# Performance work log

Measured on AMD Instinct MI355X. Metric: run time of the kernel, lower is better.

Reference implementation:

```python
import jax, jax.numpy as jnp
import numpy as np

B, S, D = 2, 512, 2048          # batch, seq, hidden
H, Dh = 16, 128                 # heads, head_dim
E, K, G, TG = 8, 2, 2, 1        # experts, top_k, n_group, topk_group
I, IS = 1024, 1024              # routed / shared expert intermediate
ROUTED_SCALE = 2.5
EPS = 1e-6
ROPE_THETA = 10000.0


def setup_inputs() -> dict:
    key = jax.random.key(0)
    ks = jax.random.split(key, 13)
    p = lambda k, shape, s=0.02: jax.random.normal(k, shape, jnp.float32) * s
    return {
        "hidden_states": jax.random.normal(ks[0], (B, S, D), jnp.float32),
        "ln1_w": jnp.ones((D,), jnp.float32),
        "ln2_w": jnp.ones((D,), jnp.float32),
        "wq": p(ks[1], (D, H * Dh)),
        "wk": p(ks[2], (D, H * Dh)),
        "wv": p(ks[3], (D, H * Dh)),
        "wo": p(ks[4], (H * Dh, D)),
        "gate_w": p(ks[5], (E, D)),
        "gate_bias": p(ks[6], (E,), 0.1),
        "w_gate": p(ks[7], (E, D, I)),
        "w_up": p(ks[8], (E, D, I)),
        "w_down": p(ks[9], (E, I, D)),
        "sw_gate": p(ks[10], (D, IS)),
        "sw_up": p(ks[11], (D, IS)),
        "sw_down": p(ks[12], (IS, D)),
    }


def _rmsnorm(x, w):
    var = jnp.mean(x * x, axis=-1, keepdims=True)
    return x * jax.lax.rsqrt(var + EPS) * w


def _rope_cos_sin(seq_len):
    inv_freq = 1.0 / (ROPE_THETA ** (jnp.arange(0, Dh, 2, dtype=jnp.float32) / Dh))
    ang = jnp.arange(seq_len, dtype=jnp.float32)[:, None] * inv_freq  # [S, Dh/2]
    return jnp.cos(ang)[None, :, None, :], jnp.sin(ang)[None, :, None, :]


def _apply_rope(x, cos, sin):
    x1, x2 = jnp.split(x, 2, axis=-1)
    return jnp.concatenate([x1 * cos - x2 * sin, x2 * cos + x1 * sin], axis=-1)


def _attention(x, wq, wk, wv, wo):
    q = (x @ wq).reshape(B, S, H, Dh)
    k = (x @ wk).reshape(B, S, H, Dh)
    v = (x @ wv).reshape(B, S, H, Dh)
    cos, sin = _rope_cos_sin(S)
    q = _apply_rope(q, cos, sin)
    k = _apply_rope(k, cos, sin)
    scores = jnp.einsum('bqhd,bkhd->bhqk', q, k) * (1.0 / np.sqrt(Dh).astype(np.float32))
    causal = jnp.tril(jnp.ones((S, S), bool))
    scores = jnp.where(causal, scores, jnp.finfo(scores.dtype).min)
    attn = jax.nn.softmax(scores, axis=-1)
    out = jnp.einsum('bhqk,bkhd->bqhd', attn, v).reshape(B, S, H * Dh)
    return out @ wo


def _moe(x, gate_w, gate_bias, w_gate, w_up, w_down, sw_gate, sw_up, sw_down):
    # x: [T, D]. noaux_tc grouped top-k routing (DeepSeek-V3 style).
    T = x.shape[0]
    logits = x @ gate_w.T                      # [T, E]
    scores = jax.nn.sigmoid(logits)
    sc = scores + gate_bias                    # selection scores with correction bias
    grp = sc.reshape(T, G, E // G)
    group_scores = jnp.sum(jax.lax.top_k(grp, 2)[0], axis=-1)  # top-2 sum per group [T,G]
    _, gidx = jax.lax.top_k(group_scores, TG)
    gmask = jnp.zeros((T, G), bool).at[jnp.arange(T)[:, None], gidx].set(True)
    emask = jnp.broadcast_to(gmask[:, :, None], (T, G, E // G)).reshape(T, E)
    masked = jnp.where(emask, sc, -jnp.inf)
    _, idx = jax.lax.top_k(masked, K)          # [T, K] expert ids
    w = jnp.take_along_axis(scores, idx, axis=-1)
    w = w / jnp.sum(w, axis=-1, keepdims=True)  # norm_topk_prob=True
    # dense combine weights [T, E] (zero except K entries per token)
    cw = jnp.zeros((T, E), x.dtype).at[jnp.arange(T)[:, None], idx].add(w)

    def body(acc, xs):
        wg, wu, wd, cwe = xs
        y = (jax.nn.silu(x @ wg) * (x @ wu)) @ wd  # SiluAndMul gated MLP
        return acc + cwe[:, None] * y, None

    routed, _ = jax.lax.scan(body, jnp.zeros_like(x), (w_gate, w_up, w_down, cw.T))
    shared = (jax.nn.silu(x @ sw_gate) * (x @ sw_up)) @ sw_down
    return routed * ROUTED_SCALE + shared


def reference(hidden_states, ln1_w, ln2_w, wq, wk, wv, wo, gate_w, gate_bias,
              w_gate, w_up, w_down, sw_gate, sw_up, sw_down):
    h = hidden_states
    h = h + _attention(_rmsnorm(h, ln1_w), wq, wk, wv, wo)
    x = _rmsnorm(h, ln2_w).reshape(B * S, D)
    moe_out = _moe(x, gate_w, gate_bias, w_gate, w_up, w_down,
                   sw_gate, sw_up, sw_down).reshape(B, S, D)
    return h + moe_out
```

## Files before the change

kernel.cpp:

```cpp
#include <hip/hip_runtime.h>

typedef __bf16 bf16x4 __attribute__((ext_vector_type(4)));
typedef __bf16 bf16x8 __attribute__((ext_vector_type(8)));
typedef float  f32x4  __attribute__((ext_vector_type(4)));

#define THREADS 256
constexpr int BK = 32, BKP = 40;

constexpr size_t MB = 1024*1024;
constexpr size_t oH2    = 0;
constexpr size_t oXB2   = 8*MB;
constexpr size_t oRT    = 12*MB;
constexpr size_t oWQKVT = 16*MB;
constexpr size_t oWQKVL = 40*MB;
constexpr size_t oWOT   = 64*MB;
constexpr size_t oWOL   = 72*MB;
constexpr size_t oXN1   = 80*MB;
constexpr size_t oXN1L  = 84*MB;
constexpr size_t oQKV   = 88*MB;
constexpr size_t oSCF   = 112*MB;
constexpr size_t oQKS   = 144*MB;
constexpr size_t oQKSL  = 152*MB;
constexpr size_t oVT    = 16*MB;
constexpr size_t oVTL   = 20*MB;
constexpr size_t oATT   = 24*MB;
constexpr size_t oPB    = 40*MB;
constexpr size_t oPBL2  = 88*MB;
constexpr size_t oWGUT  = 16*MB;
constexpr size_t oWDT   = 80*MB;
constexpr size_t oSGUT  = 112*MB;
constexpr size_t oSDT   = 120*MB;
constexpr size_t oGU    = 124*MB;
constexpr size_t oHB    = 140*MB;
constexpr size_t oY     = 144*MB;
constexpr size_t oSGU   = 16*MB;
constexpr size_t oSHB   = 24*MB;
constexpr size_t oSDB   = 26*MB;
constexpr size_t oEIDX = oRT;
constexpr size_t oEW   = oRT + 8192;
constexpr size_t oSLOT = oRT + 16384;
constexpr size_t oLIST = oRT + 24576;
constexpr size_t oCNT  = oRT + 32768;
constexpr size_t oOFF  = oRT + 33024;
constexpr size_t oCUR  = oRT + 33280;

__device__ __forceinline__ bf16x8 bzero8() {
  bf16x8 z;
#pragma unroll
  for (int j = 0; j < 8; ++j) z[j] = (__bf16)0.f;
  return z;
}

template<int OM>
__global__ void transpose_kernel(const float* __restrict__ in, __bf16* __restrict__ out,
                                 int ldin, int ldout, int zlo,
                                 long inBH, long inBL, long outB, long plane) {
  __shared__ float tile[64][65];
  int z = blockIdx.z;
  const float* inp = in + (long)(z / zlo) * inBH + (long)(z % zlo) * inBL;
  __bf16* outp = out + (long)z * outB;
  int r0 = blockIdx.y * 64, c0 = blockIdx.x * 64;
  int tid = threadIdx.x;
#pragma unroll
  for (int i = 0; i < 4; ++i) {
    int lin = tid + i * 256;
    int r = lin >> 4, c4 = (lin & 15) << 2;
    f32x4 v = *(const f32x4*)(inp + (long)(r0 + r) * ldin + c0 + c4);
    tile[r][c4] = v[0]; tile[r][c4+1] = v[1]; tile[r][c4+2] = v[2]; tile[r][c4+3] = v[3];
  }
  __syncthreads();
#pragma unroll
  for (int i = 0; i < 4; ++i) {
    int lin = tid + i * 256;
    int oR = lin >> 4, oC4 = (lin & 15) << 2;
    bf16x4 hi, lo;
#pragma unroll
    for (int j = 0; j < 4; ++j) {
      float v = tile[oC4 + j][oR];
      hi[j] = (__bf16)v;
      if constexpr (OM == 2) lo[j] = (__bf16)(v - (float)hi[j]);
    }
    __bf16* dst = outp + (long)(c0 + oR) * ldout + r0 + oC4;
    *(bf16x4*)dst = hi;
    if constexpr (OM == 2) *(bf16x4*)(dst + plane) = lo;
  }
}

template<int MODE, int SP, bool RESID, bool CAUSAL, bool KTRI, int TBM = 128, int TBN = 128>
__global__ __launch_bounds__(256, 2)
void gemm_kernel(const void* __restrict__ Av, const void* __restrict__ Bv, float* __restrict__ C,
                 const float* __restrict__ Rres,
                 int M, int N, int K, int lda, int ldb, int ldc,
                 int zlo, long aHi, long aLo, long bHi, long bLo, long cHi, long cLo,
                 long aPlane, long bPlane,
                 const int* __restrict__ counts, const int* __restrict__ offsets,
                 const int* __restrict__ gather) {
  const int n0 = blockIdx.x * TBN;
  const int m0 = blockIdx.y * TBM;
  const int z  = blockIdx.z;
  if (CAUSAL && n0 > m0) return;

  const float*  Af = (const float*)Av;
  const __bf16* Ah = (const __bf16*)Av;
  const __bf16* Bh = (const __bf16*)Bv;

  int mcount; int rowbase = 0;
  long aoff = 0, boff = 0, coff = 0;
  if constexpr (MODE == 0) {
    mcount = M;
    int zh = z / zlo, zl = z % zlo;
    aoff = (long)zh*aHi + (long)zl*aLo;
    boff = (long)zh*bHi + (long)zl*bLo;
    coff = (long)zh*cHi + (long)zl*cLo;
  } else {
    mcount = counts[z];
    rowbase = offsets[z];
    if (m0 >= mcount) return;
    boff = (long)z*bHi;
  }

  constexpr bool TRI = (SP != 0);
  constexpr int ABUF = TBM*BKP;
  constexpr int BBUF = TBN*BKP;
  constexpr int WTM = TBM/2, WTN = TBN/2;
  constexpr int MI = WTM/16, MJ = WTN/16;
  __shared__ __align__(16) __bf16 As[(TRI?2:1)*ABUF];
  __shared__ __align__(16) __bf16 Bs[(TRI?2:1)*BBUF];

  const int tid = threadIdx.x;
  const int lane = tid & 63, wave = tid >> 6;
  const int wm = wave >> 1, wn = wave & 1;
  const int lq = lane >> 4, lr = lane & 15;

  int kend = K;
  if (KTRI) { int ke = m0 + TBM; kend = ke < K ? ke : K; }

  f32x4 acc[MI][MJ] = {};

  constexpr int NAF = (SP==1) ? TBM/32 : 1;
  constexpr int NAH = (SP!=1) ? TBM/64 : 1;
  constexpr int NB  = TBN/64;
  f32x4  arf[NAF];
  bf16x8 arh[NAH], arl[NAH];
  bf16x8 brh[NB],  brl[NB];

  auto loadAB = [&](int kk) {
    if constexpr (SP == 1) {
#pragma unroll
      for (int it = 0; it < NAF; ++it) {
        int lin = tid + it*THREADS;
        int row = lin >> 3, c4 = (lin & 7) << 2;
        int gr = m0 + row;
        f32x4 zv; zv[0]=0.f; zv[1]=0.f; zv[2]=0.f; zv[3]=0.f;
        arf[it] = (gr < mcount) ? *(const f32x4*)(Af + aoff + (long)gr*lda + kk + c4) : zv;
      }
    } else {
#pragma unroll
      for (int it = 0; it < NAH; ++it) {
        int lin = tid + it*THREADS;
        int row = lin >> 2, c8 = (lin & 3) << 3;
        int gr = m0 + row;
        arh[it] = bzero8();
        if constexpr (SP == 2) arl[it] = bzero8();
        if (gr < mcount) {
          long arow;
          if constexpr (MODE == 1) arow = gather[rowbase + gr];
          else if constexpr (MODE == 2) arow = rowbase + gr;
          else arow = gr;
          const __bf16* p = Ah + aoff + arow*(long)lda + kk + c8;
          arh[it] = *(const bf16x8*)p;
          if constexpr (SP == 2) arl[it] = *(const bf16x8*)(p + aPlane);
        }
      }
    }
#pragma unroll
    for (int it = 0; it < NB; ++it) {
      int lin = tid + it*THREADS;
      int row = lin >> 2, c8 = (lin & 3) << 3;
      const __bf16* p = Bh + boff + (long)(n0+row)*ldb + kk + c8;
      brh[it] = *(const bf16x8*)p;
      if constexpr (TRI) brl[it] = *(const bf16x8*)(p + bPlane);
    }
  };

  auto writeAB = [&]() {
    if constexpr (SP == 1) {
#pragma unroll
      for (int it = 0; it < NAF; ++it) {
        int lin = tid + it*THREADS;
        int row = lin >> 3, c4 = (lin & 7) << 2;
        bf16x4 hi, lo;
#pragma unroll
        for (int j = 0; j < 4; ++j) {
          hi[j] = (__bf16)arf[it][j];
          lo[j] = (__bf16)(arf[it][j] - (float)hi[j]);
        }
        *(bf16x4*)(As + row*BKP + c4) = hi;
        *(bf16x4*)(As + ABUF + row*BKP + c4) = lo;
      }
    } else {
#pragma unroll
      for (int it = 0; it < NAH; ++it) {
        int lin = tid + it*THREADS;
        int row = lin >> 2, c8 = (lin & 3) << 3;
        *(bf16x8*)(As + row*BKP + c8) = arh[it];
        if constexpr (SP == 2) *(bf16x8*)(As + ABUF + row*BKP + c8) = arl[it];
      }
    }
#pragma unroll
    for (int it = 0; it < NB; ++it) {
      int lin = tid + it*THREADS;
      int row = lin >> 2, c8 = (lin & 3) << 3;
      *(bf16x8*)(Bs + row*BKP + c8) = brh[it];
      if constexpr (TRI) *(bf16x8*)(Bs + BBUF + row*BKP + c8) = brl[it];
    }
  };

  loadAB(0);
  writeAB();
  __syncthreads();

  for (int k0 = 0; k0 < kend; k0 += BK) {
    const bool hn = (k0 + BK < kend);
    if (hn) loadAB(k0 + BK);

    bf16x8 fa[MI], fal[MI];
    const __bf16* ap = As + (wm*WTM + lr)*BKP + lq*8;
    const __bf16* bp = Bs + (wn*WTN + lr)*BKP + lq*8;
#pragma unroll
    for (int i = 0; i < MI; ++i) {
      fa[i] = *(const bf16x8*)(ap + i*16*BKP);
      if constexpr (TRI) fal[i] = *(const bf16x8*)(ap + ABUF + i*16*BKP);
    }
#pragma unroll
    for (int j = 0; j < MJ; ++j) {
      bf16x8 fb = *(const bf16x8*)(bp + j*16*BKP);
      if constexpr (TRI) {
        bf16x8 fbl = *(const bf16x8*)(bp + BBUF + j*16*BKP);
#pragma unroll
        for (int i = 0; i < MI; ++i) {
          acc[i][j] = __builtin_amdgcn_mfma_f32_16x16x32_bf16(fa[i],  fbl, acc[i][j], 0, 0, 0);
          acc[i][j] = __builtin_amdgcn_mfma_f32_16x16x32_bf16(fal[i], fb,  acc[i][j], 0, 0, 0);
          acc[i][j] = __builtin_amdgcn_mfma_f32_16x16x32_bf16(fa[i],  fb,  acc[i][j], 0, 0, 0);
        }
      } else {
#pragma unroll
        for (int i = 0; i < MI; ++i)
          acc[i][j] = __builtin_amdgcn_mfma_f32_16x16x32_bf16(fa[i], fb, acc[i][j], 0, 0, 0);
      }
    }

    if (hn) {
      __syncthreads();
      writeAB();
      __syncthreads();
    }
  }

#pragma unroll
  for (int i = 0; i < MI; ++i) {
#pragma unroll
    for (int rg = 0; rg < 4; ++rg) {
      int lrow = wm*WTM + i*16 + lq*4 + rg;
      int gr = m0 + lrow;
      if (gr < mcount) {
        long crow = coff + (long)(rowbase + gr)*ldc;
#pragma unroll
        for (int j = 0; j < MJ; ++j) {
          int col = n0 + wn*WTN + j*16 + lr;
          float val = acc[i][j][rg];
          if constexpr (RESID) val += Rres[(long)gr*ldc + col];
          C[crow + col] = val;
        }
      }
    }
  }
}

template<int OM>
__global__ void rmsnorm_kernel(const float* __restrict__ x, const float* __restrict__ w,
                               __bf16* __restrict__ out, long plane) {
  const int row = blockIdx.x;
  const float* xr = x + (long)row * 2048;
  float ss = 0.f;
  for (int d = threadIdx.x; d < 2048; d += 256) { float v = xr[d]; ss += v*v; }
  __shared__ float red[4];
  int lane = threadIdx.x & 63, wave = threadIdx.x >> 6;
#pragma unroll
  for (int off = 32; off; off >>= 1) ss += __shfl_down(ss, off, 64);
  if (lane == 0) red[wave] = ss;
  __syncthreads();
  float tot = red[0] + red[1] + red[2] + red[3];
  float rs = rsqrtf(tot * (1.f/2048.f) + 1e-6f);
  __bf16* orow = out + (long)row * 2048;
  for (int d = threadIdx.x; d < 2048; d += 256) {
    float v = xr[d]*rs*w[d];
    __bf16 h = (__bf16)v;
    orow[d] = h;
    if constexpr (OM == 2) orow[d + plane] = (__bf16)(v - (float)h);
  }
}

__global__ void rope_split_kernel(const float* __restrict__ qkv, __bf16* __restrict__ o, long plane) {
  int tid = blockIdx.x*256 + threadIdx.x;
  int i = tid & 63;
  int th = tid >> 6;
  int h = th & 15;
  int t = th >> 4;
  int s = t & 511;
  long ib = (long)t*6144 + h*128;
  long ob = (long)t*4096 + h*128;
  float inv = 1.f / powf(10000.f, (float)i * (1.f/64.f));
  float ang = (float)s * inv;
  float c = cosf(ang), sn = sinf(ang);
  float q1 = qkv[ib+i], q2 = qkv[ib+64+i];
  float r1 = q1*c - q2*sn, r2 = q2*c + q1*sn;
  __bf16 h1 = (__bf16)r1, h2v = (__bf16)r2;
  o[ob+i] = h1;            o[ob+i+plane] = (__bf16)(r1 - (float)h1);
  o[ob+64+i] = h2v;        o[ob+64+i+plane] = (__bf16)(r2 - (float)h2v);
  float k1 = qkv[ib+2048+i], k2 = qkv[ib+2048+64+i];
  float s1 = k1*c - k2*sn, s2 = k2*c + k1*sn;
  __bf16 g1 = (__bf16)s1, g2 = (__bf16)s2;
  o[ob+2048+i] = g1;       o[ob+2048+i+plane] = (__bf16)(s1 - (float)g1);
  o[ob+2048+64+i] = g2;    o[ob+2048+64+i+plane] = (__bf16)(s2 - (float)g2);
}

__global__ void softmax_kernel(const float* __restrict__ sc, __bf16* __restrict__ p, long plane) {
  int r = blockIdx.x & 511;
  long bh = blockIdx.x >> 9;
  const float scale = 0.08838834764831845f;
  long base = (bh*512 + r)*512;
  int c0 = threadIdx.x, c1 = threadIdx.x + 256;
  float v0 = (c0 <= r) ? sc[base+c0]*scale : -3.0e38f;
  float v1 = (c1 <= r) ? sc[base+c1]*scale : -3.0e38f;
  float m = fmaxf(v0, v1);
  __shared__ float red[4];
  int lane = threadIdx.x & 63, wave = threadIdx.x >> 6;
#pragma unroll
  for (int off = 32; off; off >>= 1) m = fmaxf(m, __shfl_xor(m, off, 64));
  if (lane == 0) red[wave] = m;
  __syncthreads();
  m = fmaxf(fmaxf(red[0], red[1]), fmaxf(red[2], red[3]));
  __syncthreads();
  float e0 = (c0 <= r) ? expf(v0 - m) : 0.f;
  float e1 = (c1 <= r) ? expf(v1 - m) : 0.f;
  float s = e0 + e1;
#pragma unroll
  for (int off = 32; off; off >>= 1) s += __shfl_xor(s, off, 64);
  if (lane == 0) red[wave] = s;
  __syncthreads();
  s = red[0] + red[1] + red[2] + red[3];
  float inv = 1.f / s;
  float p0 = e0*inv, p1 = e1*inv;
  __bf16 h0 = (__bf16)p0, h1 = (__bf16)p1;
  p[base+c0] = h0; p[base+c0+plane] = (__bf16)(p0 - (float)h0);
  p[base+c1] = h1; p[base+c1+plane] = (__bf16)(p1 - (float)h1);
}

__global__ void zero8_kernel(int* c) { if (threadIdx.x < 8) c[threadIdx.x] = 0; }

__global__ void routing_kernel(const float* __restrict__ h2, const float* __restrict__ ln2w,
                               const float* __restrict__ gw, const float* __restrict__ gb,
                               int* __restrict__ eidx, float* __restrict__ ew,
                               int* __restrict__ counts) {
  int t = blockIdx.x;
  const float* xr = h2 + (long)t*2048;
  int lane = threadIdx.x & 63, wave = threadIdx.x >> 6;
  float ss = 0.f;
  for (int d = threadIdx.x; d < 2048; d += 256) { float v = xr[d]; ss += v*v; }
  __shared__ float red[4];
#pragma unroll
  for (int off = 32; off; off >>= 1) ss += __shfl_down(ss, off, 64);
  if (lane == 0) red[wave] = ss;
  __syncthreads();
  float rs = rsqrtf((red[0]+red[1]+red[2]+red[3]) * (1.f/2048.f) + 1e-6f);
  __shared__ float lg[8];
  for (int e = wave; e < 8; e += 4) {
    const float* wr = gw + (long)e*2048;
    float acc = 0.f;
    for (int d = lane; d < 2048; d += 64) acc += (xr[d]*rs*ln2w[d]) * wr[d];
#pragma unroll
    for (int off = 32; off; off >>= 1) acc += __shfl_down(acc, off, 64);
    if (lane == 0) lg[e] = acc;
  }
  __syncthreads();
  if (threadIdx.x == 0) {
    float sg[8], sc[8];
#pragma unroll
    for (int e = 0; e < 8; ++e) { sg[e] = 1.f/(1.f+expf(-lg[e])); sc[e] = sg[e] + gb[e]; }
    float gs[2];
#pragma unroll
    for (int g = 0; g < 2; ++g) {
      float m1 = -3e38f, m2 = -3e38f;
#pragma unroll
      for (int j = 0; j < 4; ++j) {
        float v = sc[4*g+j];
        if (v > m1) { m2 = m1; m1 = v; } else if (v > m2) m2 = v;
      }
      gs[g] = m1 + m2;
    }
    int b4 = (gs[1] > gs[0]) ? 4 : 0;
    int i1 = 0; float v1 = -3e38f;
#pragma unroll
    for (int j = 0; j < 4; ++j) if (sc[b4+j] > v1) { v1 = sc[b4+j]; i1 = j; }
    int i2 = -1; float v2 = -3e38f;
#pragma unroll
    for (int j = 0; j < 4; ++j) if (j != i1 && sc[b4+j] > v2) { v2 = sc[b4+j]; i2 = j; }
    float w1 = sg[b4+i1], w2 = sg[b4+i2], s = w1 + w2;
    eidx[t*2] = b4+i1; eidx[t*2+1] = b4+i2;
    ew[t*2] = w1/s;    ew[t*2+1] = w2/s;
    atomicAdd(&counts[b4+i1], 1); atomicAdd(&counts[b4+i2], 1);
  }
}

__global__ void scan_kernel(const int* __restrict__ counts, int* __restrict__ offsets,
                            int* __restrict__ cursors) {
  if (threadIdx.x == 0 && blockIdx.x == 0) {
    int s = 0;
    for (int e = 0; e < 8; ++e) { offsets[e] = s; s += counts[e]; cursors[e] = 0; }
    offsets[8] = s;
  }
}

__global__ void scatter_kernel(const int* __restrict__ eidx, const int* __restrict__ offsets,
                               int* __restrict__ cursors, int* __restrict__ list,
                               int* __restrict__ slot) {
  int t = blockIdx.x*256 + threadIdx.x;
  if (t < 1024) {
#pragma unroll
    for (int kk = 0; kk < 2; ++kk) {
      int e = eidx[t*2+kk];
      int pos = atomicAdd(&cursors[e], 1);
      int g = offsets[e] + pos;
      list[g] = t;
      slot[t*2+kk] = g;
    }
  }
}

__global__ void silumul_kernel(const float* __restrict__ gu, __bf16* __restrict__ o, int n) {
  int i = blockIdx.x*256 + threadIdx.x;
  if (i < n) {
    int s = i >> 10, j = i & 1023;
    float gv = gu[(long)s*2048 + j];
    float uv = gu[(long)s*2048 + 1024 + j];
    float sg = gv / (1.f + expf(-gv));
    o[i] = (__bf16)(sg * uv);
  }
}

__global__ void combine_kernel(const float* __restrict__ h2, const float* __restrict__ y,
                               const float* __restrict__ sdown, const int* __restrict__ slot,
                               const float* __restrict__ ew, float* __restrict__ out) {
  int i = blockIdx.x*256 + threadIdx.x;
  int t = i >> 11;
  int d = i & 2047;
  float rv = ew[t*2]   * y[(long)slot[t*2]  *2048 + d]
           + ew[t*2+1] * y[(long)slot[t*2+1]*2048 + d];
  out[i] = h2[i] + sdown[i] + 2.5f * rv;
}

extern "C" void kernel_launch(void* const* d_in, const int* in_sizes, int n_in,
                              void* d_out, int out_size, void* d_ws, size_t ws_size,
                              hipStream_t stream) {
  const float* hid  = (const float*)d_in[0];
  const float* ln1  = (const float*)d_in[1];
  const float* ln2  = (const float*)d_in[2];
  const float* wq   = (const float*)d_in[3];
  const float* wk   = (const float*)d_in[4];
  const float* wv   = (const float*)d_in[5];
  const float* wo   = (const float*)d_in[6];
  const float* gw   = (const float*)d_in[7];
  const float* gb   = (const float*)d_in[8];
  const float* wgat = (const float*)d_in[9];
  const float* wup  = (const float*)d_in[10];
  const float* wdn  = (const float*)d_in[11];
  const float* swg  = (const float*)d_in[12];
  const float* swu  = (const float*)d_in[13];
  const float* swd  = (const float*)d_in[14];
  float* out = (float*)d_out;
  char* ws = (char*)d_ws;

  float*  h2    = (float*)(ws + oH2);
  __bf16* xb2   = (__bf16*)(ws + oXB2);
  __bf16* wqkvT = (__bf16*)(ws + oWQKVT);
  __bf16* woT   = (__bf16*)(ws + oWOT);
  __bf16* xn1   = (__bf16*)(ws + oXN1);
  float*  qkv   = (float*)(ws + oQKV);
  float*  scf   = (float*)(ws + oSCF);
  __bf16* qks   = (__bf16*)(ws + oQKS);
  __bf16* vtb   = (__bf16*)(ws + oVT);
  float*  att   = (float*)(ws + oATT);
  __bf16* pb    = (__bf16*)(ws + oPB);
  __bf16* wgut  = (__bf16*)(ws + oWGUT);
  __bf16* wdt   = (__bf16*)(ws + oWDT);
  __bf16* sgut  = (__bf16*)(ws + oSGUT);
  __bf16* sdt   = (__bf16*)(ws + oSDT);
  float*  gu    = (float*)(ws + oGU);
  __bf16* hb    = (__bf16*)(ws + oHB);
  float*  ybuf  = (float*)(ws + oY);
  float*  sgu   = (float*)(ws + oSGU);
  __bf16* shb   = (__bf16*)(ws + oSHB);
  float*  sdb   = (float*)(ws + oSDB);
  int*   eidx = (int*)(ws + oEIDX);
  float* ew   = (float*)(ws + oEW);
  int*   slot = (int*)(ws + oSLOT);
  int*   list = (int*)(ws + oLIST);
  int*   cnt  = (int*)(ws + oCNT);
  int*   offs = (int*)(ws + oOFF);
  int*   curs = (int*)(ws + oCUR);

  const long S22 = (long)2048*2048, S21 = (long)2048*1024;
  const long pWQKV = (oWQKVL - oWQKVT) / 2;
  const long pWO   = (oWOL - oWOT) / 2;
  const long pXN1  = 2*MB;
  const long pQKS  = (oQKSL - oQKS) / 2;
  const long pVT   = 2*MB;
  const long pPB   = (oPBL2 - oPB) / 2;

  transpose_kernel<2><<<dim3(32,32,1), 256, 0, stream>>>(wq, wqkvT,          2048, 2048, 1, 0, 0, 0, pWQKV);
  transpose_kernel<2><<<dim3(32,32,1), 256, 0, stream>>>(wk, wqkvT + S22,    2048, 2048, 1, 0, 0, 0, pWQKV);
  transpose_kernel<2><<<dim3(32,32,1), 256, 0, stream>>>(wv, wqkvT + 2*S22,  2048, 2048, 1, 0, 0, 0, pWQKV);
  transpose_kernel<2><<<dim3(32,32,1), 256, 0, stream>>>(wo, woT,            2048, 2048, 1, 0, 0, 0, pWO);

  rmsnorm_kernel<2><<<1024, 256, 0, stream>>>(hid, ln1, xn1, pXN1);

  gemm_kernel<0, 2, false, false, false, 64, 128><<<dim3(48,16,1), 256, 0, stream>>>(
      xn1, wqkvT, qkv, nullptr, 1024, 6144, 2048, 2048, 2048, 6144,
      1, 0, 0, 0, 0, 0, 0, pXN1, pWQKV, nullptr, nullptr, nullptr);

  rope_split_kernel<<<4096, 256, 0, stream>>>(qkv, qks, pQKS);

  transpose_kernel<2><<<dim3(2,8,32), 256, 0, stream>>>(
      qkv + 4096, vtb, 6144, 512, 16, (long)512*6144, 128, (long)128*512, pVT);

  gemm_kernel<0, 2, false, true, false, 64, 64><<<dim3(8,8,32), 256, 0, stream>>>(
      qks, qks + 2048, scf, nullptr, 512, 512, 128, 4096, 4096, 512,
      16, (long)512*4096, 128, (long)512*4096, 128, (long)16*512*512, (long)512*512,
      pQKS, pQKS, nullptr, nullptr, nullptr);

  softmax_kernel<<<16384, 256, 0, stream>>>(scf, pb, pPB);

  gemm_kernel<0, 2, false, false, true, 64, 64><<<dim3(2,8,32), 256, 0, stream>>>(
      pb, vtb, att, nullptr, 512, 128, 512, 512, 512, 2048,
      16, (long)16*512*512, (long)512*512, (long)16*128*512, (long)128*512,
      (long)512*2048, 128, pPB, pVT, nullptr, nullptr, nullptr);

  gemm_kernel<0, 1, true, false, false, 64, 64><<<dim3(32,16,1), 256, 0, stream>>>(
      att, woT, h2, hid, 1024, 2048, 2048, 2048, 2048, 2048,
      1, 0, 0, 0, 0, 0, 0, 0, pWO, nullptr, nullptr, nullptr);

  rmsnorm_kernel<1><<<1024, 256, 0, stream>>>(h2, ln2, xb2, 0);
  zero8_kernel<<<1, 64, 0, stream>>>(cnt);
  routing_kernel<<<1024, 256, 0, stream>>>(h2, ln2, gw, gb, eidx, ew, cnt);
  scan_kernel<<<1, 64, 0, stream>>>(cnt, offs, curs);
  scatter_kernel<<<4, 256, 0, stream>>>(eidx, offs, curs, list, slot);

  transpose_kernel<1><<<dim3(16,32,8), 256, 0, stream>>>(wgat, wgut,        1024, 2048, 1, S21, 0, S22, 0);
  transpose_kernel<1><<<dim3(16,32,8), 256, 0, stream>>>(wup,  wgut + S21,  1024, 2048, 1, S21, 0, S22, 0);
  transpose_kernel<1><<<dim3(32,16,8), 256, 0, stream>>>(wdn,  wdt,         2048, 1024, 1, S21, 0, S21, 0);
  transpose_kernel<1><<<dim3(16,32,1), 256, 0, stream>>>(swg,  sgut,        1024, 2048, 1, 0, 0, 0, 0);
  transpose_kernel<1><<<dim3(16,32,1), 256, 0, stream>>>(swu,  sgut + S21,  1024, 2048, 1, 0, 0, 0, 0);
  transpose_kernel<1><<<dim3(32,16,1), 256, 0, stream>>>(swd,  sdt,         2048, 1024, 1, 0, 0, 0, 0);

  gemm_kernel<1, 0, false, false, false, 64, 64><<<dim3(32,16,8), 256, 0, stream>>>(
      xb2, wgut, gu, nullptr, 1024, 2048, 2048, 2048, 2048, 2048,
      1, 0, 0, S22, 0, 0, 0, 0, 0, cnt, offs, list);
  silumul_kernel<<<8192, 256, 0, stream>>>(gu, hb, 2048*1024);
  gemm_kernel<2, 0, false, false, false, 64, 64><<<dim3(32,16,8), 256, 0, stream>>>(
      hb, wdt, ybuf, nullptr, 1024, 2048, 1024, 1024, 1024, 2048,
      1, 0, 0, S21, 0, 0, 0, 0, 0, cnt, offs, nullptr);

  gemm_kernel<0, 0, false, false, false, 64, 64><<<dim3(32,16,1), 256, 0, stream>>>(
      xb2, sgut, sgu, nullptr, 1024, 2048, 2048, 2048, 2048, 2048,
      1, 0, 0, 0, 0, 0, 0, 0, 0, nullptr, nullptr, nullptr);
  silumul_kernel<<<4096, 256, 0, stream>>>(sgu, shb, 1024*1024);
  gemm_kernel<0, 0, false, false, false, 64, 64><<<dim3(32,16,1), 256, 0, stream>>>(
      shb, sdt, sdb, nullptr, 1024, 2048, 1024, 1024, 1024, 2048,
      1, 0, 0, 0, 0, 0, 0, 0, 0, nullptr, nullptr, nullptr);

  combine_kernel<<<8192, 256, 0, stream>>>(h2, ybuf, sdb, slot, ew, out);
}
```

Before: 760.1 us.

## Double-buffer global prefetch registers two tiles ahead and hoist row address math

The GEMM main loop now holds two register stage sets and issues global loads two K-tiles ahead, alternating between them, so each load has more time to complete before its LDS write. Per-row base addresses, gather indices and bounds checks are computed once before the loop instead of on every load. This adds register pressure, since two copies of the staging registers are live, which may lower occupancy or cause spills, especially for the TRI/split variants.

```diff
diff --git a/kernel.cpp b/kernel.cpp
--- a/kernel.cpp
+++ b/kernel.cpp
@@ -140,50 +140,72 @@
   constexpr int NAF = (SP==1) ? TBM/32 : 1;
   constexpr int NAH = (SP!=1) ? TBM/64 : 1;
   constexpr int NB  = TBN/64;
-  f32x4  arf[NAF];
-  bf16x8 arh[NAH], arl[NAH];
-  bf16x8 brh[NB],  brl[NB];
-
-  auto loadAB = [&](int kk) {
+  constexpr int NAR = (SP==1) ? NAF : NAH;
+
+  struct StageRegs {
+    f32x4  arf[NAF];
+    bf16x8 arh[NAH], arl[NAH];
+    bf16x8 brh[NB],  brl[NB];
+  };
+  StageRegs s0, s1;
+
+  long aBase[NAR]; bool aOK[NAR];
+#pragma unroll
+  for (int it = 0; it < NAR; ++it) {
+    int lin = tid + it*THREADS;
+    int row = (SP==1) ? (lin >> 3) : (lin >> 2);
+    int gr = m0 + row;
+    aOK[it] = gr < mcount;
+    long arow = 0;
+    if (aOK[it]) {
+      if constexpr (MODE == 1) arow = gather[rowbase + gr];
+      else if constexpr (MODE == 2) arow = rowbase + gr;
+      else arow = gr;
+    }
+    aBase[it] = aoff + arow*(long)lda;
+  }
+  long bBase[NB];
+#pragma unroll
+  for (int it = 0; it < NB; ++it) {
+    int lin = tid + it*THREADS;
+    int row = lin >> 2;
+    bBase[it] = boff + (long)(n0+row)*ldb;
+  }
+
+  auto loadAB = [&](int kk, StageRegs& S) {
     if constexpr (SP == 1) {
 #pragma unroll
       for (int it = 0; it < NAF; ++it) {
         int lin = tid + it*THREADS;
-        int row = lin >> 3, c4 = (lin & 7) << 2;
-        int gr = m0 + row;
+        int c4 = (lin & 7) << 2;
         f32x4 zv; zv[0]=0.f; zv[1]=0.f; zv[2]=0.f; zv[3]=0.f;
-        arf[it] = (gr < mcount) ? *(const f32x4*)(Af + aoff + (long)gr*lda + kk + c4) : zv;
+        S.arf[it] = aOK[it] ? *(const f32x4*)(Af + aBase[it] + kk + c4) : zv;
       }
     } else {
 #pragma unroll
       for (int it = 0; it < NAH; ++it) {
         int lin = tid + it*THREADS;
-        int row = lin >> 2, c8 = (lin & 3) << 3;
-        int gr = m0 + row;
-        arh[it] = bzero8();
-        if constexpr (SP == 2) arl[it] = bzero8();
-        if (gr < mcount) {
-          long arow;
-          if constexpr (MODE == 1) arow = gather[rowbase + gr];
-          else if constexpr (MODE == 2) arow = rowbase + gr;
-          else arow = gr;
-          const __bf16* p = Ah + aoff + arow*(long)lda + kk + c8;
-          arh[it] = *(const bf16x8*)p;
-          if constexpr (SP == 2) arl[it] = *(const bf16x8*)(p + aPlane);
+        int c8 = (lin & 3) << 3;
+        S.arh[it] = bzero8();
+        if constexpr (SP == 2) S.arl[it] = bzero8();
+        if (aOK[it]) {
+          const __bf16* p = Ah + aBase[it] + kk + c8;
+          S.arh[it] = *(const bf16x8*)p;
+          if constexpr (SP == 2) S.arl[it] = *(const bf16x8*)(p + aPlane);
         }
       }
     }
 #pragma unroll
     for (int it = 0; it < NB; ++it) {
       int lin = tid + it*THREADS;
-      int row = lin >> 2, c8 = (lin & 3) << 3;
-      const __bf16* p = Bh + boff + (long)(n0+row)*ldb + kk + c8;
-      brh[it] = *(const bf16x8*)p;
-      if constexpr (TRI) brl[it] = *(const bf16x8*)(p + bPlane);
+      int c8 = (lin & 3) << 3;
+      const __bf16* p = Bh + bBase[it] + kk + c8;
+      S.brh[it] = *(const bf16x8*)p;
+      if constexpr (TRI) S.brl[it] = *(const bf16x8*)(p + bPlane);
     }
   };
 
-  auto writeAB = [&]() {
+  auto writeAB = [&](const StageRegs& S) {
     if constexpr (SP == 1) {
 #pragma unroll
       for (int it = 0; it < NAF; ++it) {
@@ -192,8 +214,8 @@
         bf16x4 hi, lo;
 #pragma unroll
         for (int j = 0; j < 4; ++j) {
-          hi[j] = (__bf16)arf[it][j];
-          lo[j] = (__bf16)(arf[it][j] - (float)hi[j]);
+          hi[j] = (__bf16)S.arf[it][j];
+          lo[j] = (__bf16)(S.arf[it][j] - (float)hi[j]);
         }
         *(bf16x4*)(As + row*BKP + c4) = hi;
         *(bf16x4*)(As + ABUF + row*BKP + c4) = lo;
@@ -203,30 +225,24 @@
       for (int it = 0; it < NAH; ++it) {
         int lin = tid + it*THREADS;
         int row = lin >> 2, c8 = (lin & 3) << 3;
-        *(bf16x8*)(As + row*BKP + c8) = arh[it];
-        if constexpr (SP == 2) *(bf16x8*)(As + ABUF + row*BKP + c8) = arl[it];
+        *(bf16x8*)(As + row*BKP + c8) = S.arh[it];
+        if constexpr (SP == 2) *(bf16x8*)(As + ABUF + row*BKP + c8) = S.arl[it];
       }
     }
 #pragma unroll
     for (int it = 0; it < NB; ++it) {
       int lin = tid + it*THREADS;
       int row = lin >> 2, c8 = (lin & 3) << 3;
-      *(bf16x8*)(Bs + row*BKP + c8) = brh[it];
-      if constexpr (TRI) *(bf16x8*)(Bs + BBUF + row*BKP + c8) = brl[it];
+      *(bf16x8*)(Bs + row*BKP + c8) = S.brh[it];
+      if constexpr (TRI) *(bf16x8*)(Bs + BBUF + row*BKP + c8) = S.brl[it];
     }
   };
 
-  loadAB(0);
-  writeAB();
-  __syncthreads();
-
-  for (int k0 = 0; k0 < kend; k0 += BK) {
-    const bool hn = (k0 + BK < kend);
-    if (hn) loadAB(k0 + BK);
-
+  const __bf16* ap = As + (wm*WTM + lr)*BKP + lq*8;
+  const __bf16* bp = Bs + (wn*WTN + lr)*BKP + lq*8;
+
+  auto computeStep = [&]() {
     bf16x8 fa[MI], fal[MI];
-    const __bf16* ap = As + (wm*WTM + lr)*BKP + lq*8;
-    const __bf16* bp = Bs + (wn*WTN + lr)*BKP + lq*8;
 #pragma unroll
     for (int i = 0; i < MI; ++i) {
       fa[i] = *(const bf16x8*)(ap + i*16*BKP);
@@ -249,12 +265,29 @@
           acc[i][j] = __builtin_amdgcn_mfma_f32_16x16x32_bf16(fa[i], fb, acc[i][j], 0, 0, 0);
       }
     }
-
-    if (hn) {
-      __syncthreads();
-      writeAB();
-      __syncthreads();
-    }
+  };
+
+  loadAB(0, s0);
+  writeAB(s0);
+  __syncthreads();
+  if (BK < kend) loadAB(BK, s1);
+
+  int k0 = 0;
+  while (true) {
+    if (k0 + 2*BK < kend) loadAB(k0 + 2*BK, s0);
+    computeStep();
+    if (k0 + BK >= kend) break;
+    __syncthreads();
+    writeAB(s1);
+    __syncthreads();
+    k0 += BK;
+    if (k0 + 2*BK < kend) loadAB(k0 + 2*BK, s1);
+    computeStep();
+    if (k0 + BK >= kend) break;
+    __syncthreads();
+    writeAB(s0);
+    __syncthreads();
+    k0 += BK;
   }
 
 #pragma unroll
```

Result: no change. 767.7 us (+1.0%).
